# Kernel tuning notes

Measured on AMD Instinct MI355X. Metric: run time of the kernel, lower is better.

The kernel has to match this reference:

```python
import jax, jax.numpy as jnp
import numpy as np

B, S, D = 2, 2048, 2048
H, KVH, HD = 16, 4, 128
E, TOPK, FF = 8, 2, 4096
EPS = 1e-6
THETA = 1000000.0


def setup_inputs() -> dict:
    key = jax.random.key(0)
    ks = jax.random.split(key, 12)
    s = 0.02
    return {
        'hidden_states': jax.random.normal(ks[0], (B, S, D), jnp.float32),
        'attention_mask': jnp.ones((B, S), dtype=bool),
        'wq': jax.random.normal(ks[1], (D, H * HD), jnp.float32) * s,
        'wk': jax.random.normal(ks[2], (D, KVH * HD), jnp.float32) * s,
        'wv': jax.random.normal(ks[3], (D, KVH * HD), jnp.float32) * s,
        'wo': jax.random.normal(ks[4], (H * HD, D), jnp.float32) * s,
        'ln1_w': jnp.ones((D,), jnp.float32),
        'ln2_w': jnp.ones((D,), jnp.float32),
        'gate_w': jax.random.normal(ks[5], (D, E), jnp.float32) * s,
        'w_gate': jax.random.normal(ks[6], (E, D, FF), jnp.float32) * s,
        'w_up': jax.random.normal(ks[7], (E, D, FF), jnp.float32) * s,
        'w_down': jax.random.normal(ks[8], (E, FF, D), jnp.float32) * s,
    }


def rms_norm(x, w):
    xf = x.astype(jnp.float32)
    var = jnp.mean(jnp.square(xf), axis=-1, keepdims=True)
    return w * (xf * jax.lax.rsqrt(var + EPS)).astype(x.dtype)


def rotate_half(x):
    x1, x2 = x[..., : x.shape[-1] // 2], x[..., x.shape[-1] // 2 :]
    return jnp.concatenate((-x2, x1), axis=-1)


def attention(x, mask, wq, wk, wv, wo):
    q = (x @ wq).reshape(B, S, H, HD)
    k = (x @ wk).reshape(B, S, KVH, HD)
    v = (x @ wv).reshape(B, S, KVH, HD)
    # RoPE (fp32 freqs, as in MixtralRotaryEmbedding)
    inv_freq = 1.0 / (THETA ** (jnp.arange(0, HD, 2, dtype=jnp.float32) / HD))
    freqs = jnp.arange(S, dtype=jnp.float32)[:, None] * inv_freq[None, :]  # [S, HD/2]
    emb = jnp.concatenate([freqs, freqs], axis=-1)  # [S, HD]
    cos = jnp.cos(emb)[None, :, None, :]  # [1,S,1,HD]
    sin = jnp.sin(emb)[None, :, None, :]
    q = q * cos + rotate_half(q) * sin
    k = k * cos + rotate_half(k) * sin
    # GQA: repeat kv heads
    k = jnp.repeat(k, H // KVH, axis=2)
    v = jnp.repeat(v, H // KVH, axis=2)
    # faithful to source: keep-mask is triu(ones, k=1) (strictly-above-diagonal)
    causal = jnp.triu(jnp.ones((S, S), dtype=bool), k=1)
    combined = mask[:, None, None, :] & causal[None, None, :, :]  # [B,1,S,S]
    neg = jnp.finfo(jnp.float32).min
    bias = jnp.where(combined, 0.0, neg).astype(jnp.float32)
    scores = jnp.einsum('bqhd,bkhd->bhqk', q, k) * (HD ** -0.5) + bias
    attn = jax.nn.softmax(scores, axis=-1)
    out = jnp.einsum('bhqk,bkhd->bqhd', attn, v).reshape(B, S, H * HD)
    return out @ wo


def moe(x, gate_w, w_gate, w_up, w_down):
    # x: [T, D]
    T = x.shape[0]
    logits = x.astype(jnp.float32) @ gate_w  # fp32 router, [T, E]
    rw = jax.nn.softmax(logits, axis=-1)
    top_w, top_i = jax.lax.top_k(rw, TOPK)
    top_w = top_w / jnp.sum(top_w, axis=-1, keepdims=True)
    w_full = jnp.zeros((T, E), jnp.float32).at[jnp.arange(T)[:, None], top_i].set(top_w)
    out = jnp.zeros_like(x)
    for e in range(E):  # small fixed expert loop
        h = jax.nn.silu(x @ w_gate[e]) * (x @ w_up[e])
        out = out + w_full[:, e, None] * (h @ w_down[e])
    return out


def reference(hidden_states, attention_mask, wq, wk, wv, wo, ln1_w, ln2_w, gate_w, w_gate, w_up, w_down):
    residual = hidden_states
    h = rms_norm(hidden_states, ln1_w)
    h = residual + attention(h, attention_mask, wq, wk, wv, wo)
    residual = h
    h = rms_norm(h, ln2_w)
    m = moe(h.reshape(-1, D), gate_w, w_gate, w_up, w_down).reshape(B, S, D)
    return residual + m
```

## Files before the change

### kernel.cpp

```cpp
#include <hip/hip_runtime.h>
#include <cstdint>
#include <cstddef>


typedef unsigned short u16;
typedef __attribute__((ext_vector_type(8))) short short8;
typedef __attribute__((ext_vector_type(8))) _Float16 half8;
typedef __attribute__((ext_vector_type(8))) __bf16 bf16x8;
typedef __attribute__((ext_vector_type(4))) float f32x4;
typedef __attribute__((ext_vector_type(4))) u16 us4;
typedef __attribute__((ext_vector_type(4))) unsigned int u32x4;

__device__ __forceinline__ u16 f2bf(float f) {
  unsigned u = __builtin_bit_cast(unsigned, f);
  u += 0x7fffu + ((u >> 16) & 1u);
  return (u16)(u >> 16);
}
__device__ __forceinline__ void splitf16(float x, float scale, u16 &hi, u16 &lo) {
  float xs = x * scale;
  _Float16 h = (_Float16)xs;
  hi = __builtin_bit_cast(u16, h);
  _Float16 l = (_Float16)(xs - (float)h);
  lo = __builtin_bit_cast(u16, l);
}
__device__ __forceinline__ f32x4 mma_bf(short8 a, short8 b, f32x4 c) {
  return __builtin_amdgcn_mfma_f32_16x16x32_bf16(
      __builtin_bit_cast(bf16x8, a), __builtin_bit_cast(bf16x8, b), c, 0, 0, 0);
}
__device__ __forceinline__ f32x4 mma_h(short8 a, short8 b, f32x4 c) {
  return __builtin_amdgcn_mfma_f32_16x16x32_f16(
      __builtin_bit_cast(half8, a), __builtin_bit_cast(half8, b), c, 0, 0, 0);
}
__device__ __forceinline__ void gl16(const u16 *g, u16 *l) {
  __builtin_amdgcn_global_load_lds(
      (const __attribute__((address_space(1))) unsigned *)g,
      (__attribute__((address_space(3))) unsigned *)l, 16, 0, 0);
}
#define SB0() __builtin_amdgcn_sched_barrier(0)

template <int OM>
__global__ __launch_bounds__(256) void k_trans(
    const float *__restrict__ src, u16 *__restrict__ d0, u16 *__restrict__ d1,
    int ld_src, int ld_dst, long long zhi, long long zlo, int zmod,
    long long dstz, int inter, float scale) {
  int z = blockIdx.z;
  src += (long long)(z / zmod) * zhi + (long long)(z % zmod) * zlo;
  d0 += (long long)z * dstz;
  if constexpr (OM == 1) d1 += (long long)z * dstz;
  int r0 = blockIdx.y * 64, c0 = blockIdx.x * 64;
  __shared__ float t[64][65];
  int tx = threadIdx.x;
  int rr = tx >> 4, cc = (tx & 15) * 4;
#pragma unroll
  for (int i = 0; i < 4; i++) {
    float4 v = *(const float4 *)(src + (size_t)(r0 + rr + i * 16) * ld_src + c0 + cc);
    t[rr + i * 16][cc] = v.x; t[rr + i * 16][cc + 1] = v.y;
    t[rr + i * 16][cc + 2] = v.z; t[rr + i * 16][cc + 3] = v.w;
  }
  __syncthreads();
#pragma unroll
  for (int i = 0; i < 4; i++) {
    int c = rr + i * 16;
    int f = c0 + c;
    int drow = (inter < 0) ? f : (((f >> 5) << 6) + (f & 31) + (inter << 5));
    size_t bo = (size_t)drow * ld_dst + r0 + cc;
    if constexpr (OM == 0) {
      us4 o;
#pragma unroll
      for (int j = 0; j < 4; j++) o[j] = f2bf(t[cc + j][c]);
      *(us4 *)(d0 + bo) = o;
    } else {
      us4 oh, ol;
#pragma unroll
      for (int j = 0; j < 4; j++) {
        u16 a, b; splitf16(t[cc + j][c], scale, a, b);
        oh[j] = a; ol[j] = b;
      }
      *(us4 *)(d0 + bo) = oh;
      *(us4 *)(d1 + bo) = ol;
    }
  }
}

__global__ __launch_bounds__(256) void k_rms(
    const float *__restrict__ x, const float *__restrict__ w,
    u16 *__restrict__ oh, u16 *__restrict__ ol, float scale16) {
  int row = blockIdx.x, tid = threadIdx.x;
  const float *xr = x + (size_t)row * 2048;
  float4 v0 = *(const float4 *)(xr + tid * 8);
  float4 v1 = *(const float4 *)(xr + tid * 8 + 4);
  float ss = v0.x * v0.x + v0.y * v0.y + v0.z * v0.z + v0.w * v0.w +
             v1.x * v1.x + v1.y * v1.y + v1.z * v1.z + v1.w * v1.w;
  __shared__ float red[256];
  red[tid] = ss;
  __syncthreads();
  for (int s = 128; s > 0; s >>= 1) {
    if (tid < s) red[tid] += red[tid + s];
    __syncthreads();
  }
  float sc = rsqrtf(red[0] * (1.0f / 2048.0f) + 1e-6f);
  float4 w0 = *(const float4 *)(w + tid * 8);
  float4 w1 = *(const float4 *)(w + tid * 8 + 4);
  float o[8] = {v0.x * sc * w0.x, v0.y * sc * w0.y, v0.z * sc * w0.z, v0.w * sc * w0.w,
                v1.x * sc * w1.x, v1.y * sc * w1.y, v1.z * sc * w1.z, v1.w * sc * w1.w};
  size_t bo = (size_t)row * 2048 + tid * 8;
  if (ol) {
    us4 h0, h1, l0, l1;
#pragma unroll
    for (int j = 0; j < 4; j++) {
      u16 a, b;
      splitf16(o[j], scale16, a, b); h0[j] = a; l0[j] = b;
      splitf16(o[j + 4], scale16, a, b); h1[j] = a; l1[j] = b;
    }
    *(us4 *)(oh + bo) = h0; *(us4 *)(oh + bo + 4) = h1;
    *(us4 *)(ol + bo) = l0; *(us4 *)(ol + bo + 4) = l1;
  } else {
    us4 a, b;
#pragma unroll
    for (int j = 0; j < 4; j++) { a[j] = f2bf(o[j]); b[j] = f2bf(o[j + 4]); }
    *(us4 *)(oh + bo) = a; *(us4 *)(oh + bo + 4) = b;
  }
}

__global__ void k_cs(float2 *__restrict__ cs) {
  int idx = blockIdx.x * 256 + threadIdx.x;
  int s = idx >> 6, i = idx & 63;
  double inv = exp2(-(double)i * (19.931568569324174 / 64.0));
  double ang = (double)s * inv;
  cs[idx] = make_float2((float)cos(ang), (float)sin(ang));
}

__global__ __launch_bounds__(256) void k_rope(
    const float *__restrict__ qkv, const float2 *__restrict__ cs,
    u16 *__restrict__ qh, u16 *__restrict__ ql,
    u16 *__restrict__ kh, u16 *__restrict__ kl) {
  int t = blockIdx.x, tid = threadIdx.x;
  int s = t & 2047;
  const float *bp = qkv + (size_t)t * 3072;
  for (int p = tid; p < 1024; p += 256) {
    int hh = p >> 6, i = p & 63;
    float2 c = cs[s * 64 + i];
    float x1 = bp[hh * 128 + i], x2 = bp[hh * 128 + 64 + i];
    float o1 = x1 * c.x - x2 * c.y, o2 = x2 * c.x + x1 * c.y;
    size_t b1 = (size_t)t * 2048 + hh * 128 + i;
    u16 a, b;
    splitf16(o1, 16.f, a, b); qh[b1] = a; ql[b1] = b;
    splitf16(o2, 16.f, a, b); qh[b1 + 64] = a; ql[b1 + 64] = b;
  }
  {
    int hh = tid >> 6, i = tid & 63;
    float2 c = cs[s * 64 + i];
    float x1 = bp[2048 + hh * 128 + i], x2 = bp[2048 + hh * 128 + 64 + i];
    float o1 = x1 * c.x - x2 * c.y, o2 = x2 * c.x + x1 * c.y;
    size_t b1 = (size_t)t * 512 + hh * 128 + i;
    u16 a, b;
    splitf16(o1, 16.f, a, b); kh[b1] = a; kl[b1] = b;
    splitf16(o2, 16.f, a, b); kh[b1 + 64] = a; kl[b1 + 64] = b;
  }
}

__global__ __launch_bounds__(512, 4) void k_attn(
    const u16 *__restrict__ qh, const u16 *__restrict__ ql,
    const u16 *__restrict__ kh, const u16 *__restrict__ kl,
    const u16 *__restrict__ vh, const u16 *__restrict__ vl,
    u16 *__restrict__ oh, u16 *__restrict__ ol) {
  const int qx = blockIdx.x, kvh = blockIdx.y, b = blockIdx.z;
  const int qt = (b == 0) ? qx : 63 - qx;
  const int q0 = qt * 32;
  const int tid = threadIdx.x, wid = tid >> 6, lane = tid & 63;
  const int hq = wid & 3, rh = wid >> 2;
  const int h = kvh * 4 + hq;
  const int lr = lane & 15, g = lane >> 4, lk = g * 8;
  const float SC = 0.08838834764831845f * 1.44269504088896341f / 256.0f;

  __shared__ alignas(16) u16 KT[2][2][4096];
  __shared__ alignas(16) u16 VT[2][2][4096];
  __shared__ alignas(16) u16 Pb[8][2][512];

  short8 qfh[4], qfl[4];
  {
    size_t qo = (size_t)(b * 2048 + q0 + rh * 16 + lr) * 2048 + h * 128 + lk;
#pragma unroll
    for (int c = 0; c < 4; c++) {
      qfh[c] = *(const short8 *)(qh + qo + c * 32);
      qfl[c] = *(const short8 *)(ql + qo + c * 32);
    }
  }
  f32x4 accO[8] = {};
  float m_r[4], lp[4];
#pragma unroll
  for (int r = 0; r < 4; r++) { m_r[r] = -3.0e38f; lp[r] = 0.f; }

  const int kv_start = q0;
  const int nIter = (2048 - kv_start) >> 5;

  const u16 *khp = kh + (size_t)(b * 2048) * 512 + kvh * 128;
  const u16 *klp = kl + (size_t)(b * 2048) * 512 + kvh * 128;
  const u16 *vhp = vh + ((size_t)(b * 4 + kvh) * 128) * 2048;
  const u16 *vlp = vl + ((size_t)(b * 4 + kvh) * 128) * 2048;

  auto stage = [&](int bf, int kv0) {
    const int c0 = wid * 64;
    const int cc = tid;
    const int krow = cc >> 4, kcol = (cc & 15) ^ (krow & 7);
    const size_t kg = (size_t)(kv0 + krow) * 512 + kcol * 8;
    gl16(khp + kg, &KT[bf][0][c0 * 8]);
    gl16(klp + kg, &KT[bf][1][c0 * 8]);
    const int vd = cc >> 2, vi = (cc & 3) ^ (vd & 3);
    const size_t vg = (size_t)vd * 2048 + kv0 + vi * 8;
    gl16(vhp + vg, &VT[bf][0][c0 * 8]);
    gl16(vlp + vg, &VT[bf][1][c0 * 8]);
  };

  stage(0, kv_start);
  __syncthreads();
  int buf = 0;
  for (int it = 0; it < nIter; it++) {
    const int kv0 = kv_start + (it << 5);
    if (it + 1 < nIter) stage(buf ^ 1, kv0 + 32);
    f32x4 s0 = {}, s1 = {};
    {
      const u16 *KhL = KT[buf][0], *KlL = KT[buf][1];
#pragma unroll
      for (int c = 0; c < 4; c++) {
        const int idx0 = lr * 128 + (((c * 4 + g) ^ (lr & 7)) << 3);
        const int idx1 = idx0 + 2048;
        short8 k0h = *(const short8 *)(KhL + idx0);
        short8 k0l = *(const short8 *)(KlL + idx0);
        short8 k1h = *(const short8 *)(KhL + idx1);
        short8 k1l = *(const short8 *)(KlL + idx1);
        s0 = mma_h(qfh[c], k0h, s0); s0 = mma_h(qfh[c], k0l, s0); s0 = mma_h(qfl[c], k0h, s0);
        s1 = mma_h(qfh[c], k1h, s1); s1 = mma_h(qfh[c], k1l, s1); s1 = mma_h(qfl[c], k1h, s1);
      }
    }
    const bool msk = (kv0 <= q0 + 31);
    float alpha[4];
#pragma unroll
    for (int r = 0; r < 4; r++) {
      float v0 = s0[r] * SC, v1 = s1[r] * SC;
      if (msk) {
        int rowq = q0 + rh * 16 + g * 4 + r;
        if (kv0 + lr <= rowq) v0 = -3.0e38f;
        if (kv0 + 16 + lr <= rowq) v1 = -3.0e38f;
      }
      float mx = fmaxf(v0, v1);
#pragma unroll
      for (int o = 1; o < 16; o <<= 1) mx = fmaxf(mx, __shfl_xor(mx, o));
      float mn = fmaxf(m_r[r], mx);
      float p0 = exp2f(v0 - mn), p1 = exp2f(v1 - mn);
      alpha[r] = exp2f(m_r[r] - mn);
      lp[r] = lp[r] * alpha[r] + (p0 + p1);
      m_r[r] = mn;
      const int prow = g * 4 + r;
      {
        int c0l = lr, c1l = 16 + lr;
        int p0i = prow * 32 + ((c0l & 7) | ((((c0l >> 3) ^ g) & 3) << 3));
        int p1i = prow * 32 + ((c1l & 7) | ((((c1l >> 3) ^ g) & 3) << 3));
        u16 x, y;
        splitf16(p0, 16.f, x, y); Pb[wid][0][p0i] = x; Pb[wid][1][p0i] = y;
        splitf16(p1, 16.f, x, y); Pb[wid][0][p1i] = x; Pb[wid][1][p1i] = y;
      }
    }
#pragma unroll
    for (int nt = 0; nt < 8; nt++) {
      f32x4 t = accO[nt];
      t[0] *= alpha[0]; t[1] *= alpha[1]; t[2] *= alpha[2]; t[3] *= alpha[3];
      accO[nt] = t;
    }
    asm volatile("s_waitcnt lgkmcnt(0)" ::: "memory");
    const int pidx = lr * 32 + (((g ^ (lr >> 2)) & 3) << 3);
    short8 pfh = *(const short8 *)(&Pb[wid][0][pidx]);
    short8 pfl = *(const short8 *)(&Pb[wid][1][pidx]);
    {
      const u16 *VhL = VT[buf][0], *VlL = VT[buf][1];
#pragma unroll
      for (int nt = 0; nt < 8; nt++) {
        const int d = nt * 16 + lr;
        const int vidx = d * 32 + (((g ^ (d & 3)) & 3) << 3);
        short8 wfh = *(const short8 *)(VhL + vidx);
        short8 wfl = *(const short8 *)(VlL + vidx);
        f32x4 t = accO[nt];
        t = mma_h(pfh, wfh, t); t = mma_h(pfh, wfl, t); t = mma_h(pfl, wfh, t);
        accO[nt] = t;
      }
    }
    __syncthreads();
    buf ^= 1;
  }
  float inv[4];
#pragma unroll
  for (int r = 0; r < 4; r++) {
    float s = lp[r];
#pragma unroll
    for (int o = 1; o < 16; o <<= 1) s += __shfl_xor(s, o);
    inv[r] = 1.0f / (s * 256.0f);
  }
#pragma unroll
  for (int nt = 0; nt < 8; nt++)
#pragma unroll
    for (int r = 0; r < 4; r++) {
      float v = accO[nt][r] * inv[r];
      size_t idx = (size_t)(b * 2048 + q0 + rh * 16 + g * 4 + r) * 2048 + h * 128 + nt * 16 + lr;
      u16 x, y; splitf16(v, 16.f, x, y);
      oh[idx] = x; ol[idx] = y;
    }
}

__global__ __launch_bounds__(256) void k_fixrow(
    const u16 *__restrict__ vh, const u16 *__restrict__ vl,
    u16 *__restrict__ oh, u16 *__restrict__ ol) {
  const int bg = blockIdx.x >> 4, dg = blockIdx.x & 15;
  const int tid = threadIdx.x, lane = tid & 63, w = tid >> 6;
  __shared__ float part[4][8];
#pragma unroll
  for (int i = 0; i < 8; i++) {
    size_t ro = ((size_t)(bg * 128 + dg * 8 + i)) * 2048 + tid * 8;
    short8 a = *(const short8 *)(vh + ro);
    short8 c = *(const short8 *)(vl + ro);
    float s = 0.f;
#pragma unroll
    for (int j = 0; j < 8; j++)
      s += (float)__builtin_bit_cast(_Float16, (u16)a[j]) +
           (float)__builtin_bit_cast(_Float16, (u16)c[j]);
#pragma unroll
    for (int o = 1; o < 64; o <<= 1) s += __shfl_xor(s, o);
    if (lane == 0) part[w][i] = s;
  }
  __syncthreads();
  if (tid < 8) {
    float tot = part[0][tid] + part[1][tid] + part[2][tid] + part[3][tid];
    float v = tot * (1.0f / 32768.0f);
    u16 x, y; splitf16(v, 16.f, x, y);
    int bb = bg >> 2, kvh = bg & 3;
#pragma unroll
    for (int hq2 = 0; hq2 < 4; hq2++) {
      size_t idx = ((size_t)(bb * 2048 + 2047)) * 2048 + (kvh * 4 + hq2) * 128 + dg * 8 + tid;
      oh[idx] = x; ol[idx] = y;
    }
  }
}

template <int MODE>
__global__ __launch_bounds__(256) void k_gemm(
    const u16 *__restrict__ Ah, const u16 *__restrict__ Al,
    const u16 *__restrict__ Bh, const u16 *__restrict__ Bl,
    int M, int N, int K, int lda, int ldb, int ldc, float descale,
    float *__restrict__ outf, const float *__restrict__ resid) {
  const int tid = threadIdx.x;
  const int wid = tid >> 6, lane = tid & 63;
  const int wr = wid >> 1, wc = wid & 1;
  const int l15 = lane & 15, l4 = lane >> 4;
  const int n0 = blockIdx.x * 128, m0 = blockIdx.y * 128;
  __shared__ alignas(16) u16 AsH[4096], BsH[4096];
  __shared__ alignas(16) u16 AsL[4096], BsL[4096];
  const int r16 = lane >> 2, c8 = (lane & 3) << 3;
  int a0 = m0 + wid * 16 + r16, a1 = a0 + 64;
  const u16 *pa0 = Ah + (size_t)a0 * lda + c8;
  const u16 *pa1 = Ah + (size_t)a1 * lda + c8;
  const int b0 = n0 + wid * 16 + r16, b1 = b0 + 64;
  const u16 *pb0 = Bh + (size_t)b0 * ldb + c8;
  const u16 *pb1 = Bh + (size_t)b1 * ldb + c8;
  const u16 *qa0 = Al + (size_t)a0 * lda + c8;
  const u16 *qa1 = Al + (size_t)a1 * lda + c8;
  const u16 *qb0 = Bl + (size_t)b0 * ldb + c8;
  const u16 *qb1 = Bl + (size_t)b1 * ldb + c8;
  u16 *sa0 = AsH + wid * 512, *sa1 = AsH + 2048 + wid * 512;
  u16 *sb0 = BsH + wid * 512, *sb1 = BsH + 2048 + wid * 512;
  f32x4 acc[4][4] = {};
  const int fa = (wr * 64 + l15) * 32 + (l4 << 3);
  const int fb = (wc * 64 + l15) * 32 + (l4 << 3);
  for (int k0 = 0; k0 < K; k0 += 32) {
    gl16(pa0 + k0, sa0); gl16(pa1 + k0, sa1);
    gl16(pb0 + k0, sb0); gl16(pb1 + k0, sb1);
    gl16(qa0 + k0, AsL + wid * 512); gl16(qa1 + k0, AsL + 2048 + wid * 512);
    gl16(qb0 + k0, BsL + wid * 512); gl16(qb1 + k0, BsL + 2048 + wid * 512);
    __syncthreads();
    short8 ah[4], bh[4], al[4], bl[4];
#pragma unroll
    for (int i = 0; i < 4; i++) ah[i] = *(const short8 *)(AsH + fa + i * 512);
#pragma unroll
    for (int i = 0; i < 4; i++) bh[i] = *(const short8 *)(BsH + fb + i * 512);
#pragma unroll
    for (int i = 0; i < 4; i++) al[i] = *(const short8 *)(AsL + fa + i * 512);
#pragma unroll
    for (int i = 0; i < 4; i++) bl[i] = *(const short8 *)(BsL + fb + i * 512);
#pragma unroll
    for (int mi = 0; mi < 4; mi++)
#pragma unroll
      for (int ni = 0; ni < 4; ni++) {
        f32x4 c = acc[mi][ni];
        c = mma_h(ah[mi], bh[ni], c);
        c = mma_h(ah[mi], bl[ni], c);
        c = mma_h(al[mi], bh[ni], c);
        acc[mi][ni] = c;
      }
    __syncthreads();
  }
#pragma unroll
  for (int mi = 0; mi < 4; mi++)
#pragma unroll
    for (int q = 0; q < 4; q++) {
      int row = m0 + wr * 64 + l4 * 4 + mi * 16 + q;
      size_t rb = (size_t)row * ldc;
#pragma unroll
      for (int ni = 0; ni < 4; ni++) {
        int col = n0 + wc * 64 + ni * 16 + l15;
        float v = acc[mi][ni][q] * descale;
        if constexpr (MODE == 1) v += resid[rb + col];
        outf[rb + col] = v;
      }
    }
}

template <int MODE>
__global__ __launch_bounds__(512, 1) void k_gemm8(
    const u16 *__restrict__ A, const u16 *__restrict__ Ball,
    int N, int K, int lda, int ldb, int ldc,
    float *__restrict__ outf, u16 *__restrict__ outh,
    const int *__restrict__ offs, const int *__restrict__ counts,
    const int *__restrict__ row_token, const float *__restrict__ row_w) {
  const int e = blockIdx.z;
  const int seg = offs[e], cnt = counts[e];
  const int m0 = blockIdx.y * 256;
  if (m0 >= cnt) return;
  const int n0 = blockIdx.x * 256;
  const u16 *B = Ball + (size_t)e * (size_t)N * (size_t)ldb;
  const int tid = threadIdx.x, wid = tid >> 6, lane = tid & 63;
  const int wr = wid >> 2, wc = wid & 3;
  const int l15 = lane & 15, l4 = lane >> 4;

  __shared__ alignas(16) u16 Ls[4][2][8192];

  const u16 *pA[2], *pB[2];
#pragma unroll
  for (int j = 0; j < 2; j++) {
    int s = (wid * 2 + j) * 64 + lane;
    int row = s >> 2;
    int kc = (s & 3) ^ ((row >> 1) & 3);
    int ra = m0 + row; if (ra > cnt - 1) ra = cnt - 1;
    pA[j] = A + (size_t)(seg + ra) * lda + kc * 8;
    pB[j] = B + (size_t)(n0 + row) * ldb + kc * 8;
  }
  int offA[8], offB[4];
#pragma unroll
  for (int mi = 0; mi < 8; mi++) {
    int r = wr * 128 + mi * 16 + l15;
    offA[mi] = (r * 4 + (l4 ^ ((r >> 1) & 3))) << 3;
  }
#pragma unroll
  for (int ni = 0; ni < 4; ni++) {
    int r = wc * 64 + ni * 16 + l15;
    offB[ni] = (r * 4 + (l4 ^ ((r >> 1) & 3))) << 3;
  }

  f32x4 acc[8][4] = {};
  const int nT = K >> 5;
  auto stage = [&](int t, int j) {
    gl16(pA[j] + (t << 5), &Ls[t & 3][0][(wid * 2 + j) << 9]);
    gl16(pB[j] + (t << 5), &Ls[t & 3][1][(wid * 2 + j) << 9]);
  };
  stage(0, 0); stage(0, 1); stage(1, 0); stage(1, 1);
  asm volatile("s_waitcnt vmcnt(4)" ::: "memory");
  SB0();
  __builtin_amdgcn_s_barrier();
  SB0();

  short8 bf[4], af0[4], af1[4];
  for (int t = 0; t < nT; t++) {
    const u16 *LA = &Ls[t & 3][0][0], *LB = &Ls[t & 3][1][0];
#pragma unroll
    for (int i = 0; i < 4; i++) bf[i] = *(const short8 *)(LB + offB[i]);
#pragma unroll
    for (int i = 0; i < 4; i++) af0[i] = *(const short8 *)(LA + offA[i]);
    if (t + 2 < nT) stage(t + 2, 0);
    asm volatile("s_waitcnt lgkmcnt(0)" ::: "memory");
    SB0();
    __builtin_amdgcn_s_setprio(1);
#pragma unroll
    for (int mi = 0; mi < 4; mi++)
#pragma unroll
      for (int ni = 0; ni < 4; ni++)
        acc[mi][ni] = mma_bf(af0[mi], bf[ni], acc[mi][ni]);
    __builtin_amdgcn_s_setprio(0);
#pragma unroll
    for (int i = 0; i < 4; i++) af1[i] = *(const short8 *)(LA + offA[4 + i]);
    if (t + 2 < nT) stage(t + 2, 1);
    asm volatile("s_waitcnt lgkmcnt(0)" ::: "memory");
    SB0();
    __builtin_amdgcn_s_setprio(1);
#pragma unroll
    for (int mi = 0; mi < 4; mi++)
#pragma unroll
      for (int ni = 0; ni < 4; ni++)
        acc[4 + mi][ni] = mma_bf(af1[mi], bf[ni], acc[4 + mi][ni]);
    __builtin_amdgcn_s_setprio(0);
    if (t + 1 < nT) {
      if (t + 2 < nT) {
        asm volatile("s_waitcnt vmcnt(4)" ::: "memory");
      } else {
        asm volatile("s_waitcnt vmcnt(0)" ::: "memory");
      }
      SB0();
      __builtin_amdgcn_s_barrier();
      SB0();
    }
  }

  if constexpr (MODE == 2) {
    const int f0 = (n0 + wc * 64) >> 1;
#pragma unroll
    for (int mi = 0; mi < 8; mi++)
#pragma unroll
      for (int q = 0; q < 4; q++) {
        int rl = m0 + wr * 128 + mi * 16 + l4 * 4 + q;
        if (rl < cnt) {
          size_t rb = (size_t)(seg + rl) * ldc;
#pragma unroll
          for (int nt = 0; nt < 2; nt++) {
            float g = acc[mi][nt][q], u = acc[mi][nt + 2][q];
            float hv = (g / (1.0f + __expf(-g))) * u;
            outh[rb + f0 + nt * 16 + l15] = f2bf(hv);
          }
        }
      }
  } else {
#pragma unroll
    for (int mi = 0; mi < 8; mi++)
#pragma unroll
      for (int q = 0; q < 4; q++) {
        int rl = m0 + wr * 128 + mi * 16 + l4 * 4 + q;
        if (rl < cnt) {
          int tok = row_token[seg + rl];
          float w = row_w[seg + rl];
          size_t rb = (size_t)tok * ldc;
#pragma unroll
          for (int ni = 0; ni < 4; ni++)
            atomicAdd(outf + rb + n0 + wc * 64 + ni * 16 + l15,
                      w * acc[mi][ni][q]);
        }
      }
  }
}

__global__ __launch_bounds__(64) void k_router(
    const float *__restrict__ hb, const float *__restrict__ w2,
    const float *__restrict__ gw, int *__restrict__ topi,
    float *__restrict__ topw, int *__restrict__ counts) {
  const int t = blockIdx.x, lane = threadIdx.x;
  const float *xr = hb + (size_t)t * 2048;
  float xs[32];
  float ss = 0.f;
#pragma unroll
  for (int c = 0; c < 8; c++) {
    float4 v = *(const float4 *)(xr + c * 256 + lane * 4);
    xs[c * 4 + 0] = v.x; xs[c * 4 + 1] = v.y; xs[c * 4 + 2] = v.z; xs[c * 4 + 3] = v.w;
    ss += v.x * v.x + v.y * v.y + v.z * v.z + v.w * v.w;
  }
#pragma unroll
  for (int o = 1; o < 64; o <<= 1) ss += __shfl_xor(ss, o);
  const float sc = rsqrtf(ss * (1.0f / 2048.0f) + 1e-6f);
  float acc[8] = {0, 0, 0, 0, 0, 0, 0, 0};
#pragma unroll
  for (int c = 0; c < 8; c++)
#pragma unroll
    for (int j = 0; j < 4; j++) {
      int d = c * 256 + lane * 4 + j;
      float xn = xs[c * 4 + j] * sc * w2[d];
      float4 g0 = *(const float4 *)(gw + (size_t)d * 8);
      float4 g1 = *(const float4 *)(gw + (size_t)d * 8 + 4);
      acc[0] += xn * g0.x; acc[1] += xn * g0.y; acc[2] += xn * g0.z; acc[3] += xn * g0.w;
      acc[4] += xn * g1.x; acc[5] += xn * g1.y; acc[6] += xn * g1.z; acc[7] += xn * g1.w;
    }
#pragma unroll
  for (int e = 0; e < 8; e++) {
    float v = acc[e];
#pragma unroll
    for (int o = 1; o < 64; o <<= 1) v += __shfl_xor(v, o);
    acc[e] = v;
  }
  if (lane == 0) {
    float mx = acc[0];
#pragma unroll
    for (int e = 1; e < 8; e++) mx = fmaxf(mx, acc[e]);
    float p[8];
#pragma unroll
    for (int e = 0; e < 8; e++) p[e] = __expf(acc[e] - mx);
    int e0 = 0;
#pragma unroll
    for (int e = 1; e < 8; e++) if (p[e] > p[e0]) e0 = e;
    int e1 = (e0 == 0) ? 1 : 0;
#pragma unroll
    for (int e = 0; e < 8; e++) if (e != e0 && p[e] > p[e1]) e1 = e;
    float s2 = p[e0] + p[e1];
    topi[t * 2] = e0; topi[t * 2 + 1] = e1;
    topw[t * 2] = p[e0] / s2; topw[t * 2 + 1] = p[e1] / s2;
    atomicAdd(counts + e0, 1);
    atomicAdd(counts + e1, 1);
  }
}

__global__ void k_zero(int *__restrict__ p) {
  if (threadIdx.x < 8) p[threadIdx.x] = 0;
}
__global__ void k_offsets(const int *__restrict__ counts, int *__restrict__ offs,
                          int *__restrict__ cursors) {
  if (threadIdx.x == 0) {
    int o = 0;
    for (int e = 0; e < 8; e++) { offs[e] = o; o += counts[e]; cursors[e] = 0; }
    offs[8] = o;
  }
}
__global__ __launch_bounds__(256) void k_scatter(
    const int *__restrict__ topi, const float *__restrict__ topw,
    const int *__restrict__ offs, int *__restrict__ cursors,
    int *__restrict__ row_token, float *__restrict__ row_w) {
  int t = blockIdx.x * 256 + threadIdx.x;
  if (t >= 4096) return;
#pragma unroll
  for (int s = 0; s < 2; s++) {
    int e = topi[t * 2 + s];
    int pos = offs[e] + atomicAdd(cursors + e, 1);
    row_token[pos] = t;
    row_w[pos] = topw[t * 2 + s];
  }
}
__global__ __launch_bounds__(256) void k_gather(
    const u16 *__restrict__ h2, const int *__restrict__ row_token,
    u16 *__restrict__ xg) {
  int r = blockIdx.x;
  int t = row_token[r];
  ((u32x4 *)(xg + (size_t)r * 2048))[threadIdx.x] =
      ((const u32x4 *)(h2 + (size_t)t * 2048))[threadIdx.x];
}

extern "C" void kernel_launch(void *const *d_in, const int *in_sizes, int n_in,
                              void *d_out, int out_size, void *d_ws,
                              size_t ws_size, hipStream_t stream) {
  const float *hidden = (const float *)d_in[0];
  const float *wq = (const float *)d_in[2];
  const float *wk = (const float *)d_in[3];
  const float *wv = (const float *)d_in[4];
  const float *wo = (const float *)d_in[5];
  const float *ln1 = (const float *)d_in[6];
  const float *ln2 = (const float *)d_in[7];
  const float *gw = (const float *)d_in[8];
  const float *wg = (const float *)d_in[9];
  const float *wu = (const float *)d_in[10];
  const float *wd = (const float *)d_in[11];
  float *out = (float *)d_out;

  char *base = (char *)d_ws;
  size_t off = 0;
  auto alloc = [&](size_t bytes) -> char * {
    char *p = base + off;
    off += (bytes + 255) & ~(size_t)255;
    return p;
  };
  u16 *wqkvTh = (u16 *)alloc((size_t)3072 * 2048 * 2);
  u16 *wqkvTl = (u16 *)alloc((size_t)3072 * 2048 * 2);
  u16 *woTh = (u16 *)alloc((size_t)2048 * 2048 * 2);
  u16 *woTl = (u16 *)alloc((size_t)2048 * 2048 * 2);
  u16 *wguT = (u16 *)alloc((size_t)8 * 8192 * 2048 * 2);
  u16 *wdT = (u16 *)alloc((size_t)8 * 2048 * 4096 * 2);
  u16 *h1h = (u16 *)alloc((size_t)4096 * 2048 * 2);
  u16 *h1l = (u16 *)alloc((size_t)4096 * 2048 * 2);
  float *qkv = (float *)alloc((size_t)4096 * 3072 * 4);
  u16 *qbh = (u16 *)alloc((size_t)4096 * 2048 * 2);
  u16 *qbl = (u16 *)alloc((size_t)4096 * 2048 * 2);
  u16 *kbh = (u16 *)alloc((size_t)4096 * 512 * 2);
  u16 *kbl = (u16 *)alloc((size_t)4096 * 512 * 2);
  u16 *vth = (u16 *)alloc((size_t)8 * 128 * 2048 * 2);
  u16 *vtl = (u16 *)alloc((size_t)8 * 128 * 2048 * 2);
  float2 *cs = (float2 *)alloc((size_t)2048 * 64 * 8);
  u16 *aoh = (u16 *)alloc((size_t)4096 * 2048 * 2);
  u16 *aol = (u16 *)alloc((size_t)4096 * 2048 * 2);
  u16 *h2 = (u16 *)alloc((size_t)4096 * 2048 * 2);
  int *topi = (int *)alloc(4096 * 2 * 4);
  float *topwt = (float *)alloc(4096 * 2 * 4);
  int *counts = (int *)alloc(64 * 4);
  int *offs = (int *)alloc(64 * 4);
  int *cursors = (int *)alloc(64 * 4);
  int *row_token = (int *)alloc(8192 * 4);
  float *row_w = (float *)alloc(8192 * 4);
  u16 *xg = (u16 *)alloc((size_t)8192 * 2048 * 2);
  u16 *Hb = (u16 *)alloc((size_t)8192 * 4096 * 2);
  if (off > ws_size) return;

  dim3 T256(256), T64(64);
  k_cs<<<dim3(512), T256, 0, stream>>>(cs);
  k_trans<1><<<dim3(32, 32, 1), T256, 0, stream>>>(wq, wqkvTh, wqkvTl, 2048, 2048, 0, 0, 1, 0, -1, 256.f);
  k_trans<1><<<dim3(8, 32, 1), T256, 0, stream>>>(wk, wqkvTh + (size_t)2048 * 2048, wqkvTl + (size_t)2048 * 2048, 512, 2048, 0, 0, 1, 0, -1, 256.f);
  k_trans<1><<<dim3(8, 32, 1), T256, 0, stream>>>(wv, wqkvTh + (size_t)2560 * 2048, wqkvTl + (size_t)2560 * 2048, 512, 2048, 0, 0, 1, 0, -1, 256.f);
  k_trans<1><<<dim3(32, 32, 1), T256, 0, stream>>>(wo, woTh, woTl, 2048, 2048, 0, 0, 1, 0, -1, 256.f);
  k_trans<0><<<dim3(64, 32, 8), T256, 0, stream>>>(wg, wguT, nullptr, 4096, 2048, (long long)2048 * 4096, 0, 1, (long long)8192 * 2048, 0, 1.f);
  k_trans<0><<<dim3(64, 32, 8), T256, 0, stream>>>(wu, wguT, nullptr, 4096, 2048, (long long)2048 * 4096, 0, 1, (long long)8192 * 2048, 1, 1.f);
  k_trans<0><<<dim3(32, 64, 8), T256, 0, stream>>>(wd, wdT, nullptr, 2048, 4096, (long long)4096 * 2048, 0, 1, (long long)2048 * 4096, -1, 1.f);
  k_rms<<<dim3(4096), T256, 0, stream>>>(hidden, ln1, h1h, h1l, 16.f);
  k_gemm<0><<<dim3(24, 32, 1), T256, 0, stream>>>(
      h1h, h1l, wqkvTh, wqkvTl, 4096, 3072, 2048, 2048, 2048, 3072,
      1.f / 4096.f, qkv, nullptr);
  k_rope<<<dim3(4096), T256, 0, stream>>>(qkv, cs, qbh, qbl, kbh, kbl);
  k_trans<1><<<dim3(2, 32, 8), T256, 0, stream>>>(qkv + 2560, vth, vtl, 3072, 2048, (long long)2048 * 3072, 128, 4, (long long)128 * 2048, -1, 16.f);
  k_attn<<<dim3(64, 4, 2), dim3(512), 0, stream>>>(qbh, qbl, kbh, kbl, vth, vtl, aoh, aol);
  k_fixrow<<<dim3(128), T256, 0, stream>>>(vth, vtl, aoh, aol);
  k_gemm<1><<<dim3(16, 32, 1), T256, 0, stream>>>(
      aoh, aol, woTh, woTl, 4096, 2048, 2048, 2048, 2048, 2048,
      1.f / 4096.f, out, hidden);
  k_rms<<<dim3(4096), T256, 0, stream>>>(out, ln2, h2, nullptr, 1.f);
  k_zero<<<dim3(1), T64, 0, stream>>>(counts);
  k_router<<<dim3(4096), T64, 0, stream>>>(out, ln2, gw, topi, topwt, counts);
  k_offsets<<<dim3(1), dim3(1), 0, stream>>>(counts, offs, cursors);
  k_scatter<<<dim3(16), T256, 0, stream>>>(topi, topwt, offs, cursors, row_token, row_w);
  k_gather<<<dim3(8192), T256, 0, stream>>>(h2, row_token, xg);
  k_gemm8<2><<<dim3(32, 16, 8), dim3(512), 0, stream>>>(
      xg, wguT, 8192, 2048, 2048, 2048, 4096,
      nullptr, Hb, offs, counts, nullptr, nullptr);
  k_gemm8<3><<<dim3(8, 16, 8), dim3(512), 0, stream>>>(
      Hb, wdT, 2048, 4096, 4096, 4096, 2048,
      out, nullptr, offs, counts, row_token, row_w);
  (void)in_sizes; (void)n_in; (void)out_size;
}
```

Measured before the change: 1.505 ms.

## Restructure GEMM main loop into quadrant-split ping-pong schedule with next-tile LDS prefetch

Rewrites the bf16 MFMA main loop so each K-tile is computed as two half-B passes over both A halves. A fragments for the next tile are prefetched from LDS during the current tile, using alternating register sets unrolled by two. More workgroup barriers are added to interleave LDS reads, global staging and MFMA groups, and the vmcnt wait is tightened. The aim is to hide LDS read latency behind matrix math. The cost is extra barriers and higher register pressure, and the two-way unroll assumes an even tile count.

Measured after the change: 1.553 ms. 3.2% more time.

```diff
diff --git a/kernel.cpp b/kernel.cpp
--- a/kernel.cpp
+++ b/kernel.cpp
@@ -465,46 +465,75 @@
   __builtin_amdgcn_s_barrier();
   SB0();
 
-  short8 bf[4], af0[4], af1[4];
-  for (int t = 0; t < nT; t++) {
-    const u16 *LA = &Ls[t & 3][0][0], *LB = &Ls[t & 3][1][0];
-#pragma unroll
-    for (int i = 0; i < 4; i++) bf[i] = *(const short8 *)(LB + offB[i]);
-#pragma unroll
-    for (int i = 0; i < 4; i++) af0[i] = *(const short8 *)(LA + offA[i]);
-    if (t + 2 < nT) stage(t + 2, 0);
-    asm volatile("s_waitcnt lgkmcnt(0)" ::: "memory");
-    SB0();
-    __builtin_amdgcn_s_setprio(1);
-#pragma unroll
-    for (int mi = 0; mi < 4; mi++)
-#pragma unroll
-      for (int ni = 0; ni < 4; ni++)
-        acc[mi][ni] = mma_bf(af0[mi], bf[ni], acc[mi][ni]);
-    __builtin_amdgcn_s_setprio(0);
-#pragma unroll
-    for (int i = 0; i < 4; i++) af1[i] = *(const short8 *)(LA + offA[4 + i]);
-    if (t + 2 < nT) stage(t + 2, 1);
-    asm volatile("s_waitcnt lgkmcnt(0)" ::: "memory");
-    SB0();
-    __builtin_amdgcn_s_setprio(1);
-#pragma unroll
-    for (int mi = 0; mi < 4; mi++)
-#pragma unroll
-      for (int ni = 0; ni < 4; ni++)
-        acc[4 + mi][ni] = mma_bf(af1[mi], bf[ni], acc[4 + mi][ni]);
-    __builtin_amdgcn_s_setprio(0);
-    if (t + 1 < nT) {
-      if (t + 2 < nT) {
-        asm volatile("s_waitcnt vmcnt(4)" ::: "memory");
-      } else {
-        asm volatile("s_waitcnt vmcnt(0)" ::: "memory");
-      }
-      SB0();
-      __builtin_amdgcn_s_barrier();
-      SB0();
-    }
-  }
+  short8 aLa[4], aLb[4], aH[4], bL[2], bH[2];
+  {
+    const u16 *LA = &Ls[0][0][0], *LB = &Ls[0][1][0];
+#pragma unroll
+    for (int i = 0; i < 4; i++) aLa[i] = *(const short8 *)(LA + offA[i]);
+#pragma unroll
+    for (int i = 0; i < 2; i++) bL[i] = *(const short8 *)(LB + offB[i]);
+  }
+
+#define G8_BODY(T, CUR, NXT)                                                   \
+  {                                                                            \
+    const int t_ = (T);                                                        \
+    const u16 *LA = &Ls[t_ & 3][0][0], *LB = &Ls[t_ & 3][1][0];                \
+    const u16 *LAn = &Ls[(t_ + 1) & 3][0][0], *LBn = &Ls[(t_ + 1) & 3][1][0];  \
+                             \
+    _Pragma("unroll") for (int i = 0; i < 4; i++)                              \
+        aH[i] = *(const short8 *)(LA + offA[4 + i]);                           \
+    _Pragma("unroll") for (int i = 0; i < 2; i++)                              \
+        bH[i] = *(const short8 *)(LB + offB[2 + i]);                           \
+    if (t_ + 2 < nT) stage(t_ + 2, 0);                                         \
+    SB0();                                                                     \
+    __builtin_amdgcn_s_barrier();                                              \
+    asm volatile("s_waitcnt lgkmcnt(0)" ::: "memory");                         \
+    SB0();                                                                     \
+    __builtin_amdgcn_s_setprio(1);                                             \
+    _Pragma("unroll") for (int mi = 0; mi < 4; mi++)                           \
+        _Pragma("unroll") for (int ni = 0; ni < 2; ni++)                       \
+            acc[mi][ni] = mma_bf(CUR[mi], bL[ni], acc[mi][ni]);                \
+    _Pragma("unroll") for (int mi = 0; mi < 4; mi++)                           \
+        _Pragma("unroll") for (int ni = 0; ni < 2; ni++)                       \
+            acc[4 + mi][ni] = mma_bf(aH[mi], bL[ni], acc[4 + mi][ni]);         \
+    __builtin_amdgcn_s_setprio(0);                                             \
+    SB0();                                                                     \
+    if (t_ + 1 < nT) {                                                         \
+      if (t_ + 2 < nT) asm volatile("s_waitcnt vmcnt(2)" ::: "memory");        \
+      else             asm volatile("s_waitcnt vmcnt(0)" ::: "memory");        \
+    }                                                                          \
+    SB0();                                                                     \
+    __builtin_amdgcn_s_barrier();                                              \
+                            \
+    if (t_ + 1 < nT) {                                                         \
+      _Pragma("unroll") for (int i = 0; i < 4; i++)                            \
+          NXT[i] = *(const short8 *)(LAn + offA[i]);                           \
+      _Pragma("unroll") for (int i = 0; i < 2; i++)                            \
+          bL[i] = *(const short8 *)(LBn + offB[i]);                            \
+    }                                                                          \
+    if (t_ + 2 < nT) stage(t_ + 2, 1);                                         \
+    SB0();                                                                     \
+    __builtin_amdgcn_s_barrier();                                              \
+    asm volatile("s_waitcnt lgkmcnt(0)" ::: "memory");                         \
+    SB0();                                                                     \
+    __builtin_amdgcn_s_setprio(1);                                             \
+    _Pragma("unroll") for (int mi = 0; mi < 4; mi++)                           \
+        _Pragma("unroll") for (int ni = 0; ni < 2; ni++)                       \
+            acc[4 + mi][2 + ni] = mma_bf(aH[mi], bH[ni], acc[4 + mi][2 + ni]); \
+    _Pragma("unroll") for (int mi = 0; mi < 4; mi++)                           \
+        _Pragma("unroll") for (int ni = 0; ni < 2; ni++)                       \
+            acc[mi][2 + ni] = mma_bf(CUR[mi], bH[ni], acc[mi][2 + ni]);        \
+    __builtin_amdgcn_s_setprio(0);                                             \
+    SB0();                                                                     \
+    __builtin_amdgcn_s_barrier();                                              \
+    SB0();                                                                     \
+  }
+
+  for (int tt = 0; tt < nT; tt += 2) {
+    G8_BODY(tt, aLa, aLb)
+    G8_BODY(tt + 1, aLb, aLa)
+  }
+#undef G8_BODY
 
   if constexpr (MODE == 2) {
     const int f0 = (n0 + wc * 64) >> 1;
```

## Fuse expert weight bf16 conversion and token gather into grouped MoE GEMM

Applied to the files above, without the earlier changes.

The grouped expert GEMM now reads fp32 gate/up/down weights directly from the inputs, converts them to bf16 in registers and writes them into swizzled LDS, so the separate transpose/convert kernels and their large bf16 weight buffers are no longer needed. The gate/up GEMM also gathers activation rows through row_token instead of using a separate gather kernel and xg buffer. This removes several full passes over about 800MB of fp32 expert weights plus the bf16 rewrite. The cost is that each M-tile re-reads fp32 weights (twice the bytes of bf16) and does the conversion inside the main loop, which adds VALU and LDS-store work to the pipeline.

Measured after the change: 1.835 ms. 22.0% more time.

```diff
diff --git a/kernel.cpp b/kernel.cpp
--- a/kernel.cpp
+++ b/kernel.cpp
@@ -414,8 +414,9 @@
 
 template <int MODE>
 __global__ __launch_bounds__(512, 1) void k_gemm8(
-    const u16 *__restrict__ A, const u16 *__restrict__ Ball,
-    int N, int K, int lda, int ldb, int ldc,
+    const u16 *__restrict__ A, const float *__restrict__ Bw0,
+    const float *__restrict__ Bw1,
+    int K, int lda, int ldbf, int ldc,
     float *__restrict__ outf, u16 *__restrict__ outh,
     const int *__restrict__ offs, const int *__restrict__ counts,
     const int *__restrict__ row_token, const float *__restrict__ row_w) {
@@ -424,22 +425,43 @@
   const int m0 = blockIdx.y * 256;
   if (m0 >= cnt) return;
   const int n0 = blockIdx.x * 256;
-  const u16 *B = Ball + (size_t)e * (size_t)N * (size_t)ldb;
   const int tid = threadIdx.x, wid = tid >> 6, lane = tid & 63;
   const int wr = wid >> 2, wc = wid & 3;
   const int l15 = lane & 15, l4 = lane >> 4;
 
   __shared__ alignas(16) u16 Ls[4][2][8192];
 
-  const u16 *pA[2], *pB[2];
+  const u16 *pA[2];
 #pragma unroll
   for (int j = 0; j < 2; j++) {
     int s = (wid * 2 + j) * 64 + lane;
     int row = s >> 2;
     int kc = (s & 3) ^ ((row >> 1) & 3);
     int ra = m0 + row; if (ra > cnt - 1) ra = cnt - 1;
-    pA[j] = A + (size_t)(seg + ra) * lda + kc * 8;
-    pB[j] = B + (size_t)(n0 + row) * ldb + kc * 8;
+    long long arow;
+    if constexpr (MODE == 2) arow = row_token[seg + ra];
+    else arow = seg + ra;
+    pA[j] = A + (size_t)arow * lda + kc * 8;
+  }
+  const int kp2 = (tid & 15) * 2;
+  const int nb = (tid >> 4) * 8;
+  const float *pB;
+  {
+    int ng = n0 + nb;
+    if constexpr (MODE == 2) {
+      int stripe = ng >> 5;
+      const float *src = (stripe & 1) ? Bw1 : Bw0;
+      int f0 = ((stripe >> 1) << 5) + (ng & 31);
+      pB = src + (size_t)e * 2048 * 4096 + (size_t)kp2 * 4096 + f0;
+    } else {
+      pB = Bw0 + (size_t)e * 4096 * 2048 + (size_t)kp2 * 2048 + ng;
+    }
+  }
+  unsigned wofs[8];
+#pragma unroll
+  for (int i = 0; i < 8; i++) {
+    int n = nb + i;
+    wofs[i] = n * 32 + (((kp2 >> 3) ^ ((n >> 1) & 3)) << 3) + (kp2 & 7);
   }
   int offA[8], offB[4];
 #pragma unroll
@@ -455,12 +477,29 @@
 
   f32x4 acc[8][4] = {};
   const int nT = K >> 5;
-  auto stage = [&](int t, int j) {
+  float4 br0, br1;
+  auto stageA = [&](int t, int j) {
     gl16(pA[j] + (t << 5), &Ls[t & 3][0][(wid * 2 + j) << 9]);
-    gl16(pB[j] + (t << 5), &Ls[t & 3][1][(wid * 2 + j) << 9]);
   };
-  stage(0, 0); stage(0, 1); stage(1, 0); stage(1, 1);
-  asm volatile("s_waitcnt vmcnt(4)" ::: "memory");
+  auto loadB = [&](int t, int h) {
+    const float *p = pB + (size_t)t * 32 * ldbf + h * 4;
+    br0 = *(const float4 *)(p);
+    br1 = *(const float4 *)(p + ldbf);
+  };
+  auto writeB = [&](int t, int h) {
+    u16 *Bb = &Ls[t & 3][1][0];
+    float v0[4] = {br0.x, br0.y, br0.z, br0.w};
+    float v1[4] = {br1.x, br1.y, br1.z, br1.w};
+#pragma unroll
+    for (int i = 0; i < 4; i++) {
+      unsigned pk = (unsigned)f2bf(v0[i]) | ((unsigned)f2bf(v1[i]) << 16);
+      *((unsigned *)(Bb + wofs[h * 4 + i])) = pk;
+    }
+  };
+  loadB(0, 0); writeB(0, 0); loadB(0, 1); writeB(0, 1);
+  loadB(1, 0); writeB(1, 0); loadB(1, 1); writeB(1, 1);
+  stageA(0, 0); stageA(0, 1); stageA(1, 0); stageA(1, 1);
+  asm volatile("s_waitcnt vmcnt(2) lgkmcnt(0)" ::: "memory");
   SB0();
   __builtin_amdgcn_s_barrier();
   SB0();
@@ -472,7 +511,7 @@
     for (int i = 0; i < 4; i++) bf[i] = *(const short8 *)(LB + offB[i]);
 #pragma unroll
     for (int i = 0; i < 4; i++) af0[i] = *(const short8 *)(LA + offA[i]);
-    if (t + 2 < nT) stage(t + 2, 0);
+    if (t + 2 < nT) { loadB(t + 2, 0); stageA(t + 2, 0); }
     asm volatile("s_waitcnt lgkmcnt(0)" ::: "memory");
     SB0();
     __builtin_amdgcn_s_setprio(1);
@@ -482,9 +521,10 @@
       for (int ni = 0; ni < 4; ni++)
         acc[mi][ni] = mma_bf(af0[mi], bf[ni], acc[mi][ni]);
     __builtin_amdgcn_s_setprio(0);
+    if (t + 2 < nT) writeB(t + 2, 0);
 #pragma unroll
     for (int i = 0; i < 4; i++) af1[i] = *(const short8 *)(LA + offA[4 + i]);
-    if (t + 2 < nT) stage(t + 2, 1);
+    if (t + 2 < nT) { loadB(t + 2, 1); stageA(t + 2, 1); }
     asm volatile("s_waitcnt lgkmcnt(0)" ::: "memory");
     SB0();
     __builtin_amdgcn_s_setprio(1);
@@ -494,9 +534,10 @@
       for (int ni = 0; ni < 4; ni++)
         acc[4 + mi][ni] = mma_bf(af1[mi], bf[ni], acc[4 + mi][ni]);
     __builtin_amdgcn_s_setprio(0);
+    if (t + 2 < nT) writeB(t + 2, 1);
     if (t + 1 < nT) {
       if (t + 2 < nT) {
-        asm volatile("s_waitcnt vmcnt(4)" ::: "memory");
+        asm volatile("s_waitcnt vmcnt(2)" ::: "memory");
       } else {
         asm volatile("s_waitcnt vmcnt(0)" ::: "memory");
       }
@@ -623,14 +664,6 @@
     row_token[pos] = t;
     row_w[pos] = topw[t * 2 + s];
   }
-}
-__global__ __launch_bounds__(256) void k_gather(
-    const u16 *__restrict__ h2, const int *__restrict__ row_token,
-    u16 *__restrict__ xg) {
-  int r = blockIdx.x;
-  int t = row_token[r];
-  ((u32x4 *)(xg + (size_t)r * 2048))[threadIdx.x] =
-      ((const u32x4 *)(h2 + (size_t)t * 2048))[threadIdx.x];
 }
 
 extern "C" void kernel_launch(void *const *d_in, const int *in_sizes, int n_in,
@@ -660,8 +693,6 @@
   u16 *wqkvTl = (u16 *)alloc((size_t)3072 * 2048 * 2);
   u16 *woTh = (u16 *)alloc((size_t)2048 * 2048 * 2);
   u16 *woTl = (u16 *)alloc((size_t)2048 * 2048 * 2);
-  u16 *wguT = (u16 *)alloc((size_t)8 * 8192 * 2048 * 2);
-  u16 *wdT = (u16 *)alloc((size_t)8 * 2048 * 4096 * 2);
   u16 *h1h = (u16 *)alloc((size_t)4096 * 2048 * 2);
   u16 *h1l = (u16 *)alloc((size_t)4096 * 2048 * 2);
   float *qkv = (float *)alloc((size_t)4096 * 3072 * 4);
@@ -682,7 +713,6 @@
   int *cursors = (int *)alloc(64 * 4);
   int *row_token = (int *)alloc(8192 * 4);
   float *row_w = (float *)alloc(8192 * 4);
-  u16 *xg = (u16 *)alloc((size_t)8192 * 2048 * 2);
   u16 *Hb = (u16 *)alloc((size_t)8192 * 4096 * 2);
   if (off > ws_size) return;
 
@@ -692,9 +722,6 @@
   k_trans<1><<<dim3(8, 32, 1), T256, 0, stream>>>(wk, wqkvTh + (size_t)2048 * 2048, wqkvTl + (size_t)2048 * 2048, 512, 2048, 0, 0, 1, 0, -1, 256.f);
   k_trans<1><<<dim3(8, 32, 1), T256, 0, stream>>>(wv, wqkvTh + (size_t)2560 * 2048, wqkvTl + (size_t)2560 * 2048, 512, 2048, 0, 0, 1, 0, -1, 256.f);
   k_trans<1><<<dim3(32, 32, 1), T256, 0, stream>>>(wo, woTh, woTl, 2048, 2048, 0, 0, 1, 0, -1, 256.f);
-  k_trans<0><<<dim3(64, 32, 8), T256, 0, stream>>>(wg, wguT, nullptr, 4096, 2048, (long long)2048 * 4096, 0, 1, (long long)8192 * 2048, 0, 1.f);
-  k_trans<0><<<dim3(64, 32, 8), T256, 0, stream>>>(wu, wguT, nullptr, 4096, 2048, (long long)2048 * 4096, 0, 1, (long long)8192 * 2048, 1, 1.f);
-  k_trans<0><<<dim3(32, 64, 8), T256, 0, stream>>>(wd, wdT, nullptr, 2048, 4096, (long long)4096 * 2048, 0, 1, (long long)2048 * 4096, -1, 1.f);
   k_rms<<<dim3(4096), T256, 0, stream>>>(hidden, ln1, h1h, h1l, 16.f);
   k_gemm<0><<<dim3(24, 32, 1), T256, 0, stream>>>(
       h1h, h1l, wqkvTh, wqkvTl, 4096, 3072, 2048, 2048, 2048, 3072,
@@ -711,12 +738,11 @@
   k_router<<<dim3(4096), T64, 0, stream>>>(out, ln2, gw, topi, topwt, counts);
   k_offsets<<<dim3(1), dim3(1), 0, stream>>>(counts, offs, cursors);
   k_scatter<<<dim3(16), T256, 0, stream>>>(topi, topwt, offs, cursors, row_token, row_w);
-  k_gather<<<dim3(8192), T256, 0, stream>>>(h2, row_token, xg);
   k_gemm8<2><<<dim3(32, 16, 8), dim3(512), 0, stream>>>(
-      xg, wguT, 8192, 2048, 2048, 2048, 4096,
-      nullptr, Hb, offs, counts, nullptr, nullptr);
+      h2, wg, wu, 2048, 2048, 4096, 4096,
+      nullptr, Hb, offs, counts, row_token, nullptr);
   k_gemm8<3><<<dim3(8, 16, 8), dim3(512), 0, stream>>>(
-      Hb, wdT, 2048, 4096, 4096, 4096, 2048,
+      Hb, wd, nullptr, 4096, 4096, 2048, 2048,
       out, nullptr, offs, counts, row_token, row_w);
   (void)in_sizes; (void)n_in; (void)out_size;
 }
```
